# Performance work log

Measured on AMD Instinct MI355X. Metric: run time of the kernel, lower is better.

Reference implementation:

```python
import jax, jax.numpy as jnp
import numpy as np

# --- config constants (match init_kwargs) ---
TOP_K = 2          # num_experts_per_token
N_GROUP = 4        # num_expert_group
TOPK_GROUP = 2     # groups selected per token
SCALE = 2.5        # routed_scaling_factor
B, S, D = 2, 2048, 1024
E, F = 8, 512      # num_experts, moe_intermediate_size
SH = 1024          # shared intermediate = moe_intermediate_size * num_shared_experts


def setup_inputs() -> dict:
    key = jax.random.key(0)
    ks = jax.random.split(key, 10)
    w = 0.02
    return {
        "hidden_states": jax.random.normal(ks[0], (B, S, D), jnp.float32),
        "gate_w": jax.random.normal(ks[1], (E, D), jnp.float32) * w,
        "gate_bias": jax.random.normal(ks[2], (E,), jnp.float32) * 0.01,
        "w1": jax.random.normal(ks[3], (E, F, D), jnp.float32) * w,
        "w2": jax.random.normal(ks[4], (E, D, F), jnp.float32) * w,
        "w3": jax.random.normal(ks[5], (E, F, D), jnp.float32) * w,
        "shared_gate_w": jax.random.normal(ks[6], (SH, D), jnp.float32) * w,
        "shared_up_w": jax.random.normal(ks[7], (SH, D), jnp.float32) * w,
        "shared_down_w": jax.random.normal(ks[8], (D, SH), jnp.float32) * w,
    }


def _moe_gate(x2d, gate_w, gate_bias):
    """DeepSeek-V3 style group-limited sigmoid gate (inference path)."""
    T = x2d.shape[0]
    logits = x2d.astype(jnp.float32) @ gate_w.T.astype(jnp.float32)  # [T,E]
    scores = jax.nn.sigmoid(logits)
    sc = scores + gate_bias[None, :]                                  # e_score_correction_bias
    grp = sc.reshape(T, N_GROUP, E // N_GROUP)
    group_scores = jax.lax.top_k(grp, 2)[0].sum(-1)                   # [T,G] sum of top-2 in group
    gidx = jax.lax.top_k(group_scores, TOPK_GROUP)[1]                 # [T,topk_group]
    gmask = jnp.zeros((T, N_GROUP), sc.dtype).at[jnp.arange(T)[:, None], gidx].set(1.0)
    smask = jnp.repeat(gmask, E // N_GROUP, axis=1)                   # [T,E]
    tmp = jnp.where(smask > 0, sc, 0.0)                               # masked_fill(~mask, 0)
    tidx = jax.lax.top_k(tmp, TOP_K)[1]                               # [T,top_k]
    tw = jnp.take_along_axis(scores, tidx, axis=1)                    # weights from unbiased scores
    tw = tw / (tw.sum(-1, keepdims=True) + 1e-20)                     # moe_renormalize
    return tidx, tw * SCALE


def reference(hidden_states, gate_w, gate_bias, w1, w2, w3,
              shared_gate_w, shared_up_w, shared_down_w):
    b, s, d = hidden_states.shape
    x = hidden_states.reshape(-1, d)                                  # [T,D]
    T = x.shape[0]
    tidx, tw = _moe_gate(x, gate_w, gate_bias)
    # dense combine weights: ew[t,e] = sum_k tw[t,k] * (tidx[t,k]==e)
    ew = jnp.zeros((T, E), x.dtype).at[jnp.arange(T)[:, None], tidx].add(tw.astype(x.dtype))
    # routed experts (SwiGLU), computed per expert and combined with ew
    h = jax.nn.silu(jnp.einsum('td,efd->tef', x, w1)) * jnp.einsum('td,efd->tef', x, w3)
    y = jnp.einsum('tef,edf,te->td', h, w2, ew)
    # shared experts applied to identity
    shared = (jax.nn.silu(x @ shared_gate_w.T) * (x @ shared_up_w.T)) @ shared_down_w.T
    return (y + shared).reshape(b, s, d)
```

## Files before the change

### kernel.cpp

```cpp
#include <hip/hip_runtime.h>
#include <hip/hip_bf16.h>
#include <stdint.h>

#define T_TOK 4096
#define D_DIM 1024
#define E_NUM 8
#define F_DIM 512
#define SH_DIM 1024
#define SCALE_F 2.5f

#define BM 128
#define BN 128
#define BK 32

#define NBIG (E_NUM * F_DIM * D_DIM)
#define NSML (SH_DIM * D_DIM)
#define NCONV_CHUNKS ((3 * NBIG + 3 * NSML) / 4)
#define MAX_TILES 72

#define UP_SHARED_BLOCKS 256
#define UP_TOTAL (UP_SHARED_BLOCKS + MAX_TILES * 4)
#define DN_SHARED_BLOCKS 256
#define DN_TOTAL (DN_SHARED_BLOCKS + MAX_TILES * 8)

typedef unsigned short ushort_t;
typedef __attribute__((ext_vector_type(8))) short short8;
typedef __attribute__((ext_vector_type(4))) short short4v;
typedef __attribute__((ext_vector_type(4))) float f32x4;

#define GLL16(g, l)                                                                  \
  __builtin_amdgcn_global_load_lds(                                                  \
      (const __attribute__((address_space(1))) void*)(g),                            \
      (__attribute__((address_space(3))) void*)(l), 16, 0, 0)

__device__ inline ushort_t f2bf(float f) {
  union { float f; unsigned u; } cv; cv.f = f;
  unsigned u = cv.u;
  unsigned r = (u + 0x7FFFu + ((u >> 16) & 1u)) >> 16;
  return (ushort_t)r;
}

__global__ void gate_kernel(const float* __restrict__ x, const float* __restrict__ gw,
                            const float* __restrict__ gb, float* __restrict__ ew,
                            ushort_t* __restrict__ xb) {
  int t = blockIdx.x;
  int lane = threadIdx.x;
  const float* xr = x + (size_t)t * D_DIM;
  float xv[16];
#pragma unroll
  for (int i = 0; i < 16; i++) xv[i] = xr[lane + (i << 6)];
#pragma unroll
  for (int i = 0; i < 16; i++) xb[(size_t)t * D_DIM + lane + (i << 6)] = f2bf(xv[i]);
  float logit[E_NUM];
#pragma unroll
  for (int e = 0; e < E_NUM; e++) {
    const float* wr = gw + (size_t)e * D_DIM;
    float s = 0.f;
#pragma unroll
    for (int i = 0; i < 16; i++) s += xv[i] * wr[lane + (i << 6)];
#pragma unroll
    for (int off = 32; off; off >>= 1) s += __shfl_xor(s, off, 64);
    logit[e] = s;
  }
  if (lane == 0) {
    float scores[E_NUM], sc[E_NUM];
#pragma unroll
    for (int e = 0; e < E_NUM; e++) {
      scores[e] = 1.f / (1.f + expf(-logit[e]));
      sc[e] = scores[e] + gb[e];
    }
    float gs[4];
#pragma unroll
    for (int g = 0; g < 4; g++) gs[g] = sc[2 * g] + sc[2 * g + 1];
    int g0 = 0;
#pragma unroll
    for (int g = 1; g < 4; g++) if (gs[g] > gs[g0]) g0 = g;
    int g1 = -1;
#pragma unroll
    for (int g = 0; g < 4; g++) { if (g == g0) continue; if (g1 < 0 || gs[g] > gs[g1]) g1 = g; }
    float tmp[E_NUM];
#pragma unroll
    for (int e = 0; e < E_NUM; e++) {
      int g = e >> 1;
      tmp[e] = (g == g0 || g == g1) ? sc[e] : 0.f;
    }
    int e0 = 0;
#pragma unroll
    for (int e = 1; e < E_NUM; e++) if (tmp[e] > tmp[e0]) e0 = e;
    int e1 = -1;
#pragma unroll
    for (int e = 0; e < E_NUM; e++) { if (e == e0) continue; if (e1 < 0 || tmp[e] > tmp[e1]) e1 = e; }
    float w0 = scores[e0], w1v = scores[e1];
    float inv = SCALE_F / (w0 + w1v + 1e-20f);
    float o[E_NUM];
#pragma unroll
    for (int e = 0; e < E_NUM; e++) o[e] = 0.f;
    o[e0] = w0 * inv;
    o[e1] = w1v * inv;
#pragma unroll
    for (int e = 0; e < E_NUM; e++) ew[t * E_NUM + e] = o[e];
  }
}

__global__ void convert_kernel(const float* __restrict__ w1, const float* __restrict__ w2,
                               const float* __restrict__ w3, const float* __restrict__ sg,
                               const float* __restrict__ su, const float* __restrict__ sd,
                               ushort_t* __restrict__ w1b, ushort_t* __restrict__ w2b,
                               ushort_t* __restrict__ w3b, ushort_t* __restrict__ sgb,
                               ushort_t* __restrict__ sub, ushort_t* __restrict__ sdb) {
  size_t chunk = (size_t)blockIdx.x * blockDim.x + threadIdx.x;
  if (chunk >= (size_t)NCONV_CHUNKS) return;
  size_t idx = chunk * 4;
  const float* src; ushort_t* dst;
  if (idx < (size_t)NBIG)                    { src = w1; dst = w1b; }
  else if (idx < 2ull * NBIG)                { src = w2; dst = w2b; idx -= (size_t)NBIG; }
  else if (idx < 3ull * NBIG)                { src = w3; dst = w3b; idx -= 2ull * NBIG; }
  else if (idx < 3ull * NBIG + NSML)         { src = sg; dst = sgb; idx -= 3ull * NBIG; }
  else if (idx < 3ull * NBIG + 2ull * NSML)  { src = su; dst = sub; idx -= 3ull * NBIG + NSML; }
  else                                       { src = sd; dst = sdb; idx -= 3ull * NBIG + 2ull * NSML; }
  f32x4 v = *(const f32x4*)&src[idx];
  short4v o;
  o[0] = (short)f2bf(v[0]); o[1] = (short)f2bf(v[1]);
  o[2] = (short)f2bf(v[2]); o[3] = (short)f2bf(v[3]);
  *(short4v*)&dst[idx] = o;
}

__global__ void build_lists(const float* __restrict__ ew, int* __restrict__ counts,
                            int* __restrict__ toklist) {
  int t = blockIdx.x * blockDim.x + threadIdx.x;
  if (t >= T_TOK) return;
#pragma unroll
  for (int e = 0; e < E_NUM; e++) {
    if (ew[t * E_NUM + e] > 0.f) {
      int p = atomicAdd(&counts[e], 1);
      toklist[e * T_TOK + p] = t;
    }
  }
}

__global__ void assign_kernel(const int* __restrict__ counts, int4* __restrict__ assign,
                              int* __restrict__ meta) {
  if (threadIdx.x != 0 || blockIdx.x != 0) return;
  int total = 0, base = 0;
  for (int e = 0; e < E_NUM; e++) {
    int c = counts[e];
    int nt = (c + BM - 1) / BM;
    for (int i = 0; i < nt; i++) {
      assign[total] = make_int4(e, i, base, c);
      total++;
    }
    base += nt * BM;
  }
  meta[0] = total;
}

__global__ __launch_bounds__(256, 2)
void up_gemm(const ushort_t* __restrict__ xb,
             const ushort_t* __restrict__ sgb, const ushort_t* __restrict__ sub,
             const ushort_t* __restrict__ w1b, const ushort_t* __restrict__ w3b,
             const int* __restrict__ toklist,
             const int4* __restrict__ assign, const int* __restrict__ meta,
             ushort_t* __restrict__ hsh, ushort_t* __restrict__ hbuf) {
  __shared__ ushort_t la[BM * BK], lb1[BN * BK], lb2[BN * BK];
  __shared__ int ttok[BM];
  int bid = blockIdx.x;
  int tid = threadIdx.x, wid = tid >> 6, lane = tid & 63;

  const ushort_t *b1base, *b2base;
  ushort_t* dst;
  int n0, dstride;
  size_t rowbase;

  if (bid < UP_SHARED_BLOCKS) {
    int m0 = (bid >> 3) * BM;
    n0 = (bid & 7) * BN;
    b1base = sgb + (size_t)n0 * D_DIM;
    b2base = sub + (size_t)n0 * D_DIM;
    dst = hsh; dstride = SH_DIM; rowbase = m0;
    if (tid < BM) ttok[tid] = m0 + tid;
  } else {
    int rid = bid - UP_SHARED_BLOCKS;
    int tidx = rid >> 2;
    if (tidx >= meta[0]) return;
    int4 as = assign[tidx];
    int e = as.x, tile = as.y, sbase = as.z, cnt = as.w;
    n0 = (rid & 3) * BN;
    b1base = w1b + ((size_t)e * F_DIM + n0) * D_DIM;
    b2base = w3b + ((size_t)e * F_DIM + n0) * D_DIM;
    dst = hbuf; dstride = F_DIM; rowbase = (size_t)sbase + (size_t)tile * BM;
    if (tid < BM) {
      int idx = tile * BM + tid;
      ttok[tid] = (idx < cnt) ? toklist[e * T_TOK + idx] : -1;
    }
  }
  __syncthreads();

  int srow = (wid << 5) + (lane >> 2);
  int c16 = lane & 3;
  int s0 = c16 ^ ((srow >> 1) & 3);
  int s1 = c16 ^ (((srow + 16) >> 1) & 3);
  int tka = ttok[srow], tkb = ttok[srow + 16];
  const ushort_t* gA0 = xb + (size_t)(tka < 0 ? 0 : tka) * D_DIM + (s0 << 3);
  const ushort_t* gA1 = xb + (size_t)(tkb < 0 ? 0 : tkb) * D_DIM + (s1 << 3);
  const ushort_t* gB1a = b1base + (size_t)srow * D_DIM + (s0 << 3);
  const ushort_t* gB1b = b1base + (size_t)(srow + 16) * D_DIM + (s1 << 3);
  const ushort_t* gB2a = b2base + (size_t)srow * D_DIM + (s0 << 3);
  const ushort_t* gB2b = b2base + (size_t)(srow + 16) * D_DIM + (s1 << 3);
  ushort_t* lA0 = la + (wid << 10);
  ushort_t* lA1 = la + (wid << 10) + 512;
  ushort_t* lB1a = lb1 + (wid << 10);
  ushort_t* lB1b = lb1 + (wid << 10) + 512;
  ushort_t* lB2a = lb2 + (wid << 10);
  ushort_t* lB2b = lb2 + (wid << 10) + 512;

  int wm = (wid >> 1) << 6, wn = (wid & 1) << 6;
  int rsel = lane & 15, g = lane >> 4;
  int offA[4], offB[4];
#pragma unroll
  for (int i = 0; i < 4; i++) {
    int R = wm + i * 16 + rsel;
    offA[i] = (R << 5) + ((g ^ ((R >> 1) & 3)) << 3);
    int R2 = wn + i * 16 + rsel;
    offB[i] = (R2 << 5) + ((g ^ ((R2 >> 1) & 3)) << 3);
  }

  f32x4 acc1[4][4] = {{{0.f}}}, acc2[4][4] = {{{0.f}}};
  for (int k0 = 0; k0 < D_DIM; k0 += BK) {
    GLL16(gA0, lA0);   GLL16(gA1, lA1);
    GLL16(gB1a, lB1a); GLL16(gB1b, lB1b);
    GLL16(gB2a, lB2a); GLL16(gB2b, lB2b);
    gA0 += BK; gA1 += BK; gB1a += BK; gB1b += BK; gB2a += BK; gB2b += BK;
    __syncthreads();
    short8 af[4], bf1[4], bf2[4];
#pragma unroll
    for (int i = 0; i < 4; i++) {
      af[i]  = *(const short8*)&la[offA[i]];
      bf1[i] = *(const short8*)&lb1[offB[i]];
      bf2[i] = *(const short8*)&lb2[offB[i]];
    }
#pragma unroll
    for (int mi = 0; mi < 4; mi++)
#pragma unroll
      for (int ni = 0; ni < 4; ni++) {
        acc1[mi][ni] = __builtin_amdgcn_mfma_f32_16x16x32_bf16(af[mi], bf1[ni], acc1[mi][ni], 0, 0, 0);
        acc2[mi][ni] = __builtin_amdgcn_mfma_f32_16x16x32_bf16(af[mi], bf2[ni], acc2[mi][ni], 0, 0, 0);
      }
    __syncthreads();
  }
  int cw = lane & 15, rw = (lane >> 4) << 2;
#pragma unroll
  for (int mi = 0; mi < 4; mi++)
#pragma unroll
    for (int ni = 0; ni < 4; ni++)
#pragma unroll
      for (int r = 0; r < 4; r++) {
        int lrow = wm + mi * 16 + rw + r;
        int col = n0 + wn + ni * 16 + cw;
        float gg = acc1[mi][ni][r], u = acc2[mi][ni][r];
        float h = gg * (1.f / (1.f + __expf(-gg))) * u;
        dst[(rowbase + lrow) * (size_t)dstride + col] = f2bf(h);
      }
}

__global__ __launch_bounds__(256, 2)
void down_gemm(const ushort_t* __restrict__ hsh, const ushort_t* __restrict__ hbuf,
               const ushort_t* __restrict__ sdb, const ushort_t* __restrict__ w2b,
               const int* __restrict__ toklist, const float* __restrict__ ew,
               const int4* __restrict__ assign, const int* __restrict__ meta,
               float* __restrict__ out) {
  __shared__ ushort_t la[BM * BK], lb[BN * BK];
  __shared__ int ttok[BM];
  __shared__ float twt[BM];
  int bid = blockIdx.x;
  int tid = threadIdx.x, wid = tid >> 6, lane = tid & 63;

  const ushort_t *abase, *bbase;
  int n0, kend;

  if (bid < DN_SHARED_BLOCKS) {
    int m0 = (bid >> 3) * BM;
    n0 = (bid & 7) * BN;
    abase = hsh + (size_t)m0 * SH_DIM;
    bbase = sdb + (size_t)n0 * SH_DIM;
    kend = SH_DIM;
    if (tid < BM) { ttok[tid] = m0 + tid; twt[tid] = 1.f; }
  } else {
    int rid = bid - DN_SHARED_BLOCKS;
    int tidx = rid >> 3;
    if (tidx >= meta[0]) return;
    int4 as = assign[tidx];
    int e = as.x, tile = as.y, sbase = as.z, cnt = as.w;
    n0 = (rid & 7) * BN;
    abase = hbuf + ((size_t)sbase + (size_t)tile * BM) * F_DIM;
    bbase = w2b + ((size_t)e * D_DIM + n0) * F_DIM;
    kend = F_DIM;
    if (tid < BM) {
      int idx = tile * BM + tid;
      int tk = (idx < cnt) ? toklist[e * T_TOK + idx] : -1;
      ttok[tid] = tk;
      twt[tid] = (tk >= 0) ? ew[tk * E_NUM + e] : 0.f;
    }
  }
  __syncthreads();

  int srow = (wid << 5) + (lane >> 2);
  int c16 = lane & 3;
  int s0 = c16 ^ ((srow >> 1) & 3);
  int s1 = c16 ^ (((srow + 16) >> 1) & 3);
  const ushort_t* gA0 = abase + (size_t)srow * kend + (s0 << 3);
  const ushort_t* gA1 = abase + (size_t)(srow + 16) * kend + (s1 << 3);
  const ushort_t* gB0 = bbase + (size_t)srow * kend + (s0 << 3);
  const ushort_t* gB1 = bbase + (size_t)(srow + 16) * kend + (s1 << 3);
  ushort_t* lA0 = la + (wid << 10);
  ushort_t* lA1 = la + (wid << 10) + 512;
  ushort_t* lB0 = lb + (wid << 10);
  ushort_t* lB1 = lb + (wid << 10) + 512;

  int wm = (wid >> 1) << 6, wn = (wid & 1) << 6;
  int rsel = lane & 15, g = lane >> 4;
  int offA[4], offB[4];
#pragma unroll
  for (int i = 0; i < 4; i++) {
    int R = wm + i * 16 + rsel;
    offA[i] = (R << 5) + ((g ^ ((R >> 1) & 3)) << 3);
    int R2 = wn + i * 16 + rsel;
    offB[i] = (R2 << 5) + ((g ^ ((R2 >> 1) & 3)) << 3);
  }

  f32x4 acc[4][4] = {{{0.f}}};
  for (int k0 = 0; k0 < kend; k0 += BK) {
    GLL16(gA0, lA0); GLL16(gA1, lA1);
    GLL16(gB0, lB0); GLL16(gB1, lB1);
    gA0 += BK; gA1 += BK; gB0 += BK; gB1 += BK;
    __syncthreads();
    short8 af[4], bf[4];
#pragma unroll
    for (int i = 0; i < 4; i++) {
      af[i] = *(const short8*)&la[offA[i]];
      bf[i] = *(const short8*)&lb[offB[i]];
    }
#pragma unroll
    for (int mi = 0; mi < 4; mi++)
#pragma unroll
      for (int ni = 0; ni < 4; ni++)
        acc[mi][ni] = __builtin_amdgcn_mfma_f32_16x16x32_bf16(af[mi], bf[ni], acc[mi][ni], 0, 0, 0);
    __syncthreads();
  }
  int cw = lane & 15, rw = (lane >> 4) << 2;
#pragma unroll
  for (int mi = 0; mi < 4; mi++)
#pragma unroll
    for (int ni = 0; ni < 4; ni++)
#pragma unroll
      for (int r = 0; r < 4; r++) {
        int lrow = wm + mi * 16 + rw + r;
        int tk = ttok[lrow];
        if (tk >= 0) {
          int col = n0 + wn + ni * 16 + cw;
          atomicAdd(&out[(size_t)tk * D_DIM + col], twt[lrow] * acc[mi][ni][r]);
        }
      }
}

extern "C" void kernel_launch(void* const* d_in, const int* in_sizes, int n_in,
                              void* d_out, int out_size, void* d_ws, size_t ws_size,
                              hipStream_t stream) {
  const float* x  = (const float*)d_in[0];
  const float* gw = (const float*)d_in[1];
  const float* gb = (const float*)d_in[2];
  const float* w1 = (const float*)d_in[3];
  const float* w2 = (const float*)d_in[4];
  const float* w3 = (const float*)d_in[5];
  const float* sg = (const float*)d_in[6];
  const float* su = (const float*)d_in[7];
  const float* sd = (const float*)d_in[8];
  float* out = (float*)d_out;

  char* ws = (char*)d_ws;
  size_t off = 0;
  auto alloc = [&](size_t bytes) {
    char* p = ws + off;
    off += (bytes + 255) & ~(size_t)255;
    return p;
  };
  ushort_t* xb   = (ushort_t*)alloc((size_t)T_TOK * D_DIM * 2);
  ushort_t* w1b  = (ushort_t*)alloc((size_t)NBIG * 2);
  ushort_t* w2b  = (ushort_t*)alloc((size_t)NBIG * 2);
  ushort_t* w3b  = (ushort_t*)alloc((size_t)NBIG * 2);
  ushort_t* sgb  = (ushort_t*)alloc((size_t)NSML * 2);
  ushort_t* sub  = (ushort_t*)alloc((size_t)NSML * 2);
  ushort_t* sdb  = (ushort_t*)alloc((size_t)NSML * 2);
  float*    ew   = (float*)alloc((size_t)T_TOK * E_NUM * 4);
  ushort_t* hsh  = (ushort_t*)alloc((size_t)T_TOK * SH_DIM * 2);
  ushort_t* hbuf = (ushort_t*)alloc((size_t)MAX_TILES * BM * F_DIM * 2);
  int*      toklist = (int*)alloc((size_t)E_NUM * T_TOK * 4);
  int*      counts  = (int*)alloc(64);
  int4*     assign  = (int4*)alloc((MAX_TILES + 8) * sizeof(int4));
  int*      meta    = (int*)alloc(64);

  hipMemsetAsync(counts, 0, 64, stream);
  hipMemsetAsync(out, 0, (size_t)out_size * sizeof(float), stream);
  gate_kernel<<<T_TOK, 64, 0, stream>>>(x, gw, gb, ew, xb);
  convert_kernel<<<NCONV_CHUNKS / 256, 256, 0, stream>>>(w1, w2, w3, sg, su, sd,
                                                         w1b, w2b, w3b, sgb, sub, sdb);
  build_lists<<<(T_TOK + 255) / 256, 256, 0, stream>>>(ew, counts, toklist);
  assign_kernel<<<1, 64, 0, stream>>>(counts, assign, meta);
  up_gemm<<<UP_TOTAL, 256, 0, stream>>>(xb, sgb, sub, w1b, w3b, toklist, assign, meta,
                                        hsh, hbuf);
  down_gemm<<<DN_TOTAL, 256, 0, stream>>>(hsh, hbuf, sdb, w2b, toklist, ew, assign, meta,
                                          out);
}
```

Before: 276.7 us.

## Double-buffer LDS tiles in up and down expert GEMMs to overlap loads with MFMA

Both GEMM kernels get two LDS buffers per operand. The next K-tile is issued through global_load_lds into the idle buffer before the MFMAs on the current buffer run, so global-memory latency is hidden behind compute instead of stalling at a barrier each iteration. One barrier per iteration is removed. In exchange, LDS per block doubles (up_gemm goes to about 48KB), which could limit occupancy, and correctness depends on the end-of-iteration barrier waiting for the outstanding async loads.

```diff
diff --git a/kernel.cpp b/kernel.cpp
--- a/kernel.cpp
+++ b/kernel.cpp
@@ -12,6 +12,7 @@
 #define BM 128
 #define BN 128
 #define BK 32
+#define TILE_E (BM * BK)
 
 #define NBIG (E_NUM * F_DIM * D_DIM)
 #define NSML (SH_DIM * D_DIM)
@@ -161,7 +162,7 @@
              const int* __restrict__ toklist,
              const int4* __restrict__ assign, const int* __restrict__ meta,
              ushort_t* __restrict__ hsh, ushort_t* __restrict__ hbuf) {
-  __shared__ ushort_t la[BM * BK], lb1[BN * BK], lb2[BN * BK];
+  __shared__ ushort_t la[2 * TILE_E], lb1[2 * TILE_E], lb2[2 * TILE_E];
   __shared__ int ttok[BM];
   int bid = blockIdx.x;
   int tid = threadIdx.x, wid = tid >> 6, lane = tid & 63;
@@ -206,12 +207,8 @@
   const ushort_t* gB1b = b1base + (size_t)(srow + 16) * D_DIM + (s1 << 3);
   const ushort_t* gB2a = b2base + (size_t)srow * D_DIM + (s0 << 3);
   const ushort_t* gB2b = b2base + (size_t)(srow + 16) * D_DIM + (s1 << 3);
-  ushort_t* lA0 = la + (wid << 10);
-  ushort_t* lA1 = la + (wid << 10) + 512;
-  ushort_t* lB1a = lb1 + (wid << 10);
-  ushort_t* lB1b = lb1 + (wid << 10) + 512;
-  ushort_t* lB2a = lb2 + (wid << 10);
-  ushort_t* lB2b = lb2 + (wid << 10) + 512;
+  int wo0 = (wid << 10);
+  int wo1 = (wid << 10) + 512;
 
   int wm = (wid >> 1) << 6, wn = (wid & 1) << 6;
   int rsel = lane & 15, g = lane >> 4;
@@ -225,18 +222,29 @@
   }
 
   f32x4 acc1[4][4] = {{{0.f}}}, acc2[4][4] = {{{0.f}}};
-  for (int k0 = 0; k0 < D_DIM; k0 += BK) {
-    GLL16(gA0, lA0);   GLL16(gA1, lA1);
-    GLL16(gB1a, lB1a); GLL16(gB1b, lB1b);
-    GLL16(gB2a, lB2a); GLL16(gB2b, lB2b);
-    gA0 += BK; gA1 += BK; gB1a += BK; gB1b += BK; gB2a += BK; gB2b += BK;
-    __syncthreads();
+
+  GLL16(gA0, la + wo0);   GLL16(gA1, la + wo1);
+  GLL16(gB1a, lb1 + wo0); GLL16(gB1b, lb1 + wo1);
+  GLL16(gB2a, lb2 + wo0); GLL16(gB2b, lb2 + wo1);
+  gA0 += BK; gA1 += BK; gB1a += BK; gB1b += BK; gB2a += BK; gB2b += BK;
+  __syncthreads();
+
+  const int NT = D_DIM / BK;
+  int cur = 0;
+  for (int t = 0; t < NT; ++t) {
+    int nxt = cur ^ TILE_E;
+    if (t + 1 < NT) {
+      GLL16(gA0, la + nxt + wo0);   GLL16(gA1, la + nxt + wo1);
+      GLL16(gB1a, lb1 + nxt + wo0); GLL16(gB1b, lb1 + nxt + wo1);
+      GLL16(gB2a, lb2 + nxt + wo0); GLL16(gB2b, lb2 + nxt + wo1);
+      gA0 += BK; gA1 += BK; gB1a += BK; gB1b += BK; gB2a += BK; gB2b += BK;
+    }
     short8 af[4], bf1[4], bf2[4];
 #pragma unroll
     for (int i = 0; i < 4; i++) {
-      af[i]  = *(const short8*)&la[offA[i]];
-      bf1[i] = *(const short8*)&lb1[offB[i]];
-      bf2[i] = *(const short8*)&lb2[offB[i]];
+      af[i]  = *(const short8*)&la[cur + offA[i]];
+      bf1[i] = *(const short8*)&lb1[cur + offB[i]];
+      bf2[i] = *(const short8*)&lb2[cur + offB[i]];
     }
 #pragma unroll
     for (int mi = 0; mi < 4; mi++)
@@ -246,7 +254,9 @@
         acc2[mi][ni] = __builtin_amdgcn_mfma_f32_16x16x32_bf16(af[mi], bf2[ni], acc2[mi][ni], 0, 0, 0);
       }
     __syncthreads();
-  }
+    cur = nxt;
+  }
+
   int cw = lane & 15, rw = (lane >> 4) << 2;
 #pragma unroll
   for (int mi = 0; mi < 4; mi++)
@@ -268,7 +278,7 @@
                const int* __restrict__ toklist, const float* __restrict__ ew,
                const int4* __restrict__ assign, const int* __restrict__ meta,
                float* __restrict__ out) {
-  __shared__ ushort_t la[BM * BK], lb[BN * BK];
+  __shared__ ushort_t la[2 * TILE_E], lb[2 * TILE_E];
   __shared__ int ttok[BM];
   __shared__ float twt[BM];
   int bid = blockIdx.x;
@@ -311,10 +321,8 @@
   const ushort_t* gA1 = abase + (size_t)(srow + 16) * kend + (s1 << 3);
   const ushort_t* gB0 = bbase + (size_t)srow * kend + (s0 << 3);
   const ushort_t* gB1 = bbase + (size_t)(srow + 16) * kend + (s1 << 3);
-  ushort_t* lA0 = la + (wid << 10);
-  ushort_t* lA1 = la + (wid << 10) + 512;
-  ushort_t* lB0 = lb + (wid << 10);
-  ushort_t* lB1 = lb + (wid << 10) + 512;
+  int wo0 = (wid << 10);
+  int wo1 = (wid << 10) + 512;
 
   int wm = (wid >> 1) << 6, wn = (wid & 1) << 6;
   int rsel = lane & 15, g = lane >> 4;
@@ -328,16 +336,26 @@
   }
 
   f32x4 acc[4][4] = {{{0.f}}};
-  for (int k0 = 0; k0 < kend; k0 += BK) {
-    GLL16(gA0, lA0); GLL16(gA1, lA1);
-    GLL16(gB0, lB0); GLL16(gB1, lB1);
-    gA0 += BK; gA1 += BK; gB0 += BK; gB1 += BK;
-    __syncthreads();
+
+  GLL16(gA0, la + wo0); GLL16(gA1, la + wo1);
+  GLL16(gB0, lb + wo0); GLL16(gB1, lb + wo1);
+  gA0 += BK; gA1 += BK; gB0 += BK; gB1 += BK;
+  __syncthreads();
+
+  const int NT = kend / BK;
+  int cur = 0;
+  for (int t = 0; t < NT; ++t) {
+    int nxt = cur ^ TILE_E;
+    if (t + 1 < NT) {
+      GLL16(gA0, la + nxt + wo0); GLL16(gA1, la + nxt + wo1);
+      GLL16(gB0, lb + nxt + wo0); GLL16(gB1, lb + nxt + wo1);
+      gA0 += BK; gA1 += BK; gB0 += BK; gB1 += BK;
+    }
     short8 af[4], bf[4];
 #pragma unroll
     for (int i = 0; i < 4; i++) {
-      af[i] = *(const short8*)&la[offA[i]];
-      bf[i] = *(const short8*)&lb[offB[i]];
+      af[i] = *(const short8*)&la[cur + offA[i]];
+      bf[i] = *(const short8*)&lb[cur + offB[i]];
     }
 #pragma unroll
     for (int mi = 0; mi < 4; mi++)
@@ -345,7 +363,9 @@
       for (int ni = 0; ni < 4; ni++)
         acc[mi][ni] = __builtin_amdgcn_mfma_f32_16x16x32_bf16(af[mi], bf[ni], acc[mi][ni], 0, 0, 0);
     __syncthreads();
-  }
+    cur = nxt;
+  }
+
   int cw = lane & 15, rw = (lane >> 4) << 2;
 #pragma unroll
   for (int mi = 0; mi < 4; mi++)
```

New measurement: 293.8 us. 1.06x slower.
